# Optimization experiments

Measured on AMD Instinct MI355X. Metric: run time of the kernel, lower is better.

The kernel has to match this reference:

```python
import jax, jax.numpy as jnp
import numpy as np

B, CIN, COUT, H, W = 4, 128, 128, 128, 128
K = 3
K2 = K * K
PAD = 1
EPS = 1e-5


def setup_inputs() -> dict:
    key = jax.random.key(0)
    ks = jax.random.split(key, 11)
    def n(k, shp, s=0.05):
        return jax.random.normal(k, shp, jnp.float32) * s
    return {
        'x': jax.random.normal(ks[0], (B, CIN, H, W), jnp.float32),
        'w_attn': n(ks[1], (COUT, CIN, 3, 3)), 'b_attn': n(ks[2], (COUT,)),
        'w_feat': n(ks[3], (COUT, CIN, 3, 3)), 'b_feat': n(ks[4], (COUT,)),
        'w_org': n(ks[5], (COUT, COUT, 3, 3)), 'b_org': n(ks[6], (COUT,)),
        'w_off': n(ks[7], (2 * K2, COUT, 3, 3), 0.01), 'b_off': n(ks[8], (2 * K2,), 0.01),
        'w_mask': n(ks[9], (K2, COUT, 3, 3)), 'b_mask': n(ks[10], (K2,)),
    }


def _conv(x, w, b, stride=1, pad=1):
    y = jax.lax.conv_general_dilated(
        x, w, (stride, stride), [(pad, pad), (pad, pad)],
        dimension_numbers=('NCHW', 'OIHW', 'NCHW'))
    return y + b[None, :, None, None]


def _instance_norm(x):
    mu = jnp.mean(x, axis=(2, 3), keepdims=True)
    var = jnp.var(x, axis=(2, 3), keepdims=True)
    return (x - mu) * jax.lax.rsqrt(var + EPS)


def _lrelu(x):
    return jnp.where(x > 0, x, 0.2 * x)


def _bilinear_gather(img, y, x):
    Hin, Win = img.shape[2], img.shape[3]
    y0 = jnp.floor(y)
    x0 = jnp.floor(x)
    wy = y - y0
    wx = x - x0
    y0i = y0.astype(jnp.int32)
    x0i = x0.astype(jnp.int32)
    acc = None
    for dy, dx, w in ((0, 0, (1 - wy) * (1 - wx)), (0, 1, (1 - wy) * wx),
                      (1, 0, wy * (1 - wx)), (1, 1, wy * wx)):
        yi = y0i + dy
        xi = x0i + dx
        valid = (yi >= 0) & (yi < Hin) & (xi >= 0) & (xi < Win)
        yc = jnp.clip(yi, 0, Hin - 1)
        xc = jnp.clip(xi, 0, Win - 1)
        g = jax.vmap(lambda im, yy, xx: im[:, yy, xx])(img, yc, xc)  # [B,C,K2,H,W]
        ww = (w * valid.astype(img.dtype))[:, None]
        acc = g * ww if acc is None else acc + g * ww
    return acc


def _deform_conv(x, w_org, b_org, w_off, b_off, w_mask, b_mask):
    # torchvision-style modulated deform_conv2d, K=3, stride=1, pad=1
    b, c, h, w = x.shape
    offset = _conv(x, w_off, b_off, 1, 1)                       # [B,2*K2,H,W]
    mask = jax.nn.sigmoid(_conv(x, w_mask, b_mask, 1, 1))       # [B,K2,H,W]
    off = offset.reshape(b, K2, 2, h, w)
    dy, dx = off[:, :, 0], off[:, :, 1]
    ki = jnp.arange(K2, dtype=jnp.float32) // K                 # tap row (row-major)
    kj = jnp.arange(K2, dtype=jnp.float32) % K                  # tap col
    hh = jnp.arange(h, dtype=jnp.float32)
    wwg = jnp.arange(w, dtype=jnp.float32)
    y = dy + hh[None, None, :, None] + ki[None, :, None, None] - PAD
    xs = dx + wwg[None, None, None, :] + kj[None, :, None, None] - PAD
    samp = _bilinear_gather(x, y, xs)                           # [B,C,K2,H,W]
    samp = samp * mask[:, None]
    wflat = w_org.reshape(w_org.shape[0], c, K2)
    out = jnp.einsum('bckhw,ock->bohw', samp, wflat)
    return out + b_org[None, :, None, None]


def reference(x, w_attn, b_attn, w_feat, b_feat, w_org, b_org,
              w_off, b_off, w_mask, b_mask):
    attn = jax.nn.sigmoid(_conv(x, w_attn, b_attn, 1, 1))
    x_feat = _lrelu(_instance_norm(_conv(x, w_feat, b_feat, 1, 1)))
    x_attned = x_feat * attn
    dconv = _deform_conv(x_attned, w_org, b_org, w_off, b_off, w_mask, b_mask)
    x_valid = _lrelu(_instance_norm(dconv))
    return x_attned + x_valid * (1 - attn)
```

## Files before the change

kernel.cpp:

```cpp
#include <hip/hip_runtime.h>
#include <math.h>

#define BDIM 256
constexpr int BB = 4, Cc = 128, Hh = 128, Wd = 128, HW = Hh * Wd;
constexpr float EPSv = 1e-5f;

typedef __attribute__((ext_vector_type(8))) short short8v;
typedef __attribute__((ext_vector_type(4))) float floatx4;
typedef __attribute__((ext_vector_type(2))) float float2v;

#define MFMA16(a, b, c) __builtin_amdgcn_mfma_f32_16x16x32_bf16((a), (b), (c), 0, 0, 0)

__device__ __forceinline__ float sigmoidf_(float v) { return 1.f / (1.f + __expf(-v)); }

__device__ __forceinline__ unsigned short f2bf(float f) {
    union { float f; unsigned u; } v; v.f = f;
    unsigned r = v.u + 0x7FFFu + ((v.u >> 16) & 1u);
    return (unsigned short)(r >> 16);
}
__device__ __forceinline__ unsigned cvtpk(float a, float b) {
    unsigned r;
    asm("v_cvt_pk_bf16_f32 %0, %1, %2" : "=v"(r) : "v"(a), "v"(b));
    return r;
}
__device__ __forceinline__ float bfu(unsigned short u) { union { unsigned u; float f; } v; v.u = ((unsigned)u) << 16; return v.f; }
__device__ __forceinline__ float2v unpk2(unsigned u) {
    union { unsigned x[2]; float2v f; } v;
    v.x[0] = u << 16;
    v.x[1] = u & 0xFFFF0000u;
    return v.f;
}

__device__ __forceinline__ void barrier_lgkm() {
    asm volatile("s_waitcnt lgkmcnt(0)" ::: "memory");
    __builtin_amdgcn_s_barrier();
}

__device__ __forceinline__ void gload16(const void* g, void* l) {
    __builtin_amdgcn_global_load_lds(
        (const __attribute__((address_space(1))) unsigned int*)g,
        (__attribute__((address_space(3))) unsigned int*)l, 16, 0, 0);
}

__global__ void repack_all_k(const float* __restrict__ w_attn, const float* __restrict__ w_feat,
                             const float* __restrict__ w_org, const float* __restrict__ w_off,
                             const float* __restrict__ w_mask, const float* __restrict__ b_off,
                             const float* __restrict__ b_mask,
                             unsigned short* __restrict__ wpkAF, unsigned short* __restrict__ wpkO,
                             unsigned short* __restrict__ wpkOM, float* __restrict__ bom) {
    int idx = blockIdx.x * BDIM + threadIdx.x;
    const int TOT = 26 * 18432;
    if (idx < TOT) {
        int seg = idx / 18432, rem = idx % 18432;
        int i = rem & 7, lane = (rem >> 3) & 63, tap = (rem >> 9) % 9, chunk = rem / (9 * 512);
        int lco = lane & 15;
        int ci = chunk * 32 + (lane >> 4) * 8 + i;
        float v = 0.f;
        unsigned short* dst;
        int didx;
        if (seg < 16) {
            int cot = seg & 7;
            const float* w = (seg < 8) ? w_attn : w_feat;
            int co = cot * 16 + lco;
            v = w[((size_t)co * Cc + ci) * 9 + tap];
            dst = wpkAF; didx = idx;
        } else if (seg < 24) {
            int co = (seg - 16) * 16 + lco;
            v = w_org[((size_t)co * Cc + ci) * 9 + tap];
            dst = wpkO; didx = idx - 16 * 18432;
        } else {
            int co = (seg - 24) * 16 + lco;
            if (co < 18)      v = w_off[((size_t)co * Cc + ci) * 9 + tap];
            else if (co < 27) v = w_mask[((size_t)(co - 18) * Cc + ci) * 9 + tap];
            dst = wpkOM; didx = idx - 24 * 18432;
        }
        dst[didx] = f2bf(v);
    } else if (idx < TOT + 32) {
        int j = idx - TOT;
        bom[j] = (j < 18) ? b_off[j] : (j < 27 ? b_mask[j - 18] : 0.f);
    }
}

__global__ __launch_bounds__(256) void tobf_k(const float* __restrict__ x,
                                              unsigned short* __restrict__ dst) {
    const int h = blockIdx.x, b = blockIdx.y;
    const int t = threadIdx.x;
    __shared__ unsigned short lt[16][128];
    const int ciq = t >> 4, wg = t & 15;
    const int w = t >> 1, half = t & 1;
    for (int s = 0; s < 8; s++) {
        const float* p = x + ((size_t)(b * 128 + s * 16 + ciq) * HW + h * 128 + wg * 8);
        float4 a = *(const float4*)p;
        float4 c = *(const float4*)(p + 4);
        *(uint4*)&lt[ciq][wg * 8] =
            make_uint4(cvtpk(a.x, a.y), cvtpk(a.z, a.w), cvtpk(c.x, c.y), cvtpk(c.z, c.w));
        __syncthreads();
        unsigned r[4];
#pragma unroll
        for (int k = 0; k < 4; k++) {
            unsigned lo = lt[half * 8 + 2 * k][w];
            unsigned hi = lt[half * 8 + 2 * k + 1][w];
            r[k] = lo | (hi << 16);
        }
        *(uint4*)(dst + ((size_t)b * HW + h * 128 + w) * 128 + s * 16 + half * 8) =
            make_uint4(r[0], r[1], r[2], r[3]);
        __syncthreads();
    }
}

template <int COTPB, int WCO, bool SWZ>
__global__ __launch_bounds__(256, 2) void conv3_k(
    const unsigned short* __restrict__ src, const unsigned short* __restrict__ wpk,
    const float* __restrict__ biasA, const float* __restrict__ biasB,
    int bsplit, int sigsplit,
    unsigned short* __restrict__ out, int ldc, int ch0) {
    constexpr int ROWS = 2;
    constexpr int WPX = 4 / WCO;
    constexpr int PXW = 128 / WPX;
    constexpr int PS = PXW / 16;
    constexpr int HB = 128 / ROWS;

    const int t = threadIdx.x;
    const int lane = t & 63, llo = t & 15, lhi = (t >> 4) & 3;
    const int widu = __builtin_amdgcn_readfirstlane(t >> 6);
    const int wr = widu / WPX, wc = widu % WPX;

    int cbi, h0, b;
    if (SWZ) {
        int n = blockIdx.x;
        int xcd = n & 7, j = n >> 3;
        int g = (j >> 2) * 8 + xcd;
        cbi = j & 3;
        h0 = (g % HB) * ROWS;
        b = g / HB;
    } else {
        cbi = 0;
        h0 = ((int)blockIdx.x % HB) * ROWS;
        b = (int)blockIdx.x / HB;
    }
    const int cotbase = cbi * COTPB + wr * 2;

    __shared__ unsigned short xs[2][4][4][128][8];

    floatx4 acc[2][ROWS][PS];
#pragma unroll
    for (int c = 0; c < 2; c++)
#pragma unroll
        for (int row = 0; row < ROWS; row++)
#pragma unroll
            for (int ps = 0; ps < PS; ps++) acc[c][row][ps] = (floatx4){0.f, 0.f, 0.f, 0.f};

    const unsigned short* srcb = src + ((size_t)b * HW + (size_t)(h0 - 1) * 128) * 128;

    auto stage = [&](int chunk, int buf) {
        const unsigned short* sb = srcb + chunk * 32 + widu * 8;
        unsigned short* db = &xs[buf][widu][0][0][0];
#pragma unroll
        for (int i = 0; i < 8; i++) {
            const unsigned short* g = sb + (size_t)(i * 64 + lane) * 128;
            gload16(g, db + i * 512);
        }
    };

    short8v afrA[9][2], afrB[9][2];
    auto loadafr = [&](int chunk, short8v (*dst)[2]) {
#pragma unroll
        for (int tap = 0; tap < 9; tap++)
#pragma unroll
            for (int c = 0; c < 2; c++)
                dst[tap][c] = *(const short8v*)(wpk +
                    ((((size_t)(cotbase + c) * 4 + chunk) * 9 + tap) * 64 + lane) * 8);
    };

    stage(0, 0);
    loadafr(0, afrA);
    __syncthreads();

    const int wcb = wc * PXW;
#pragma unroll
    for (int chunk = 0; chunk < 4; ++chunk) {
        const int buf = chunk & 1;
        if (chunk < 3) {
            stage(chunk + 1, buf ^ 1);
            loadafr(chunk + 1, (chunk & 1) ? afrA : afrB);
        }
        short8v (*cur)[2] = (chunk & 1) ? afrB : afrA;
#pragma unroll
        for (int rowr = 0; rowr < ROWS + 2; ++rowr) {
            const int hh = h0 - 1 + rowr;
            if ((unsigned)hh < 128u) {
#pragma unroll
                for (int dx = 0; dx < 3; ++dx) {
#pragma unroll
                    for (int ps = 0; ps < PS; ps++) {
                        int colr = wcb + ps * 16 + llo + dx - 1;
                        int colc = min(max(colr, 0), 127);
                        short8v bfv = *(const short8v*)&xs[buf][lhi][rowr][colc][0];
                        if (colr != colc) bfv = (short8v)(short)0;
#pragma unroll
                        for (int row = 0; row < ROWS; ++row) {
                            const int r = rowr - row;
                            if (r >= 0 && r < 3) {
                                const int tap = r * 3 + dx;
#pragma unroll
                                for (int c = 0; c < 2; c++)
                                    acc[c][row][ps] = MFMA16(cur[tap][c], bfv, acc[c][row][ps]);
                            }
                        }
                    }
                }
            }
        }
        __syncthreads();
    }

    const int cbase = cbi * (COTPB * 16);
    const float* bp = (cbase < bsplit) ? biasA : biasB;
    const int bshift = (cbase < bsplit) ? 0 : bsplit;
    const bool dosig = cbase < sigsplit;
#pragma unroll
    for (int c = 0; c < 2; c++)
#pragma unroll
        for (int row = 0; row < ROWS; row++)
#pragma unroll
            for (int ps = 0; ps < PS; ps++)
#pragma unroll
                for (int reg = 0; reg < 4; reg++) {
                    int co = cbase + (wr * 2 + c) * 16 + lhi * 4 + reg;
                    int px = wc * PXW + ps * 16 + llo;
                    float v = acc[c][row][ps][reg] + bp[co - bshift];
                    if (dosig) v = sigmoidf_(v);
                    out[((size_t)b * ldc + ch0 + co) * HW + (h0 + row) * Wd + px] = f2bf(v);
                }
}

__global__ __launch_bounds__(256) void inorm_stats_k(const unsigned short* __restrict__ src,
                                                     float* __restrict__ mu, float* __restrict__ rsig,
                                                     int chTot, int ch0) {
    const int bc = blockIdx.x;
    const int b = bc >> 7, c = bc & 127;
    const unsigned short* p = src + ((size_t)b * chTot + ch0 + c) * HW;
    float s = 0.f, s2 = 0.f;
    for (int i = threadIdx.x; i < HW / 8; i += BDIM) {
        uint4 v = *(const uint4*)(p + (size_t)i * 8);
        float2v a = unpk2(v.x), bb = unpk2(v.y), cc = unpk2(v.z), dd = unpk2(v.w);
        s += a[0] + a[1] + bb[0] + bb[1] + cc[0] + cc[1] + dd[0] + dd[1];
        s2 += a[0] * a[0] + a[1] * a[1] + bb[0] * bb[0] + bb[1] * bb[1]
            + cc[0] * cc[0] + cc[1] * cc[1] + dd[0] * dd[0] + dd[1] * dd[1];
    }
    __shared__ float ss[BDIM], sq[BDIM];
    int t = threadIdx.x;
    ss[t] = s; sq[t] = s2;
    __syncthreads();
    for (int off = BDIM / 2; off > 0; off >>= 1) {
        if (t < off) { ss[t] += ss[t + off]; sq[t] += sq[t + off]; }
        __syncthreads();
    }
    if (t == 0) {
        float m = ss[0] / HW;
        float var = sq[0] / HW - m * m;
        mu[bc] = m;
        rsig[bc] = rsqrtf(var + EPSv);
    }
}

__global__ __launch_bounds__(256) void xattned2_k(const unsigned short* __restrict__ rawAF,
                                                  const float* __restrict__ mu,
                                                  const float* __restrict__ rsig,
                                                  unsigned short* __restrict__ xabfG) {
    const int seg = blockIdx.x, h = blockIdx.y, b = blockIdx.z;
    const int t = threadIdx.x;
    __shared__ unsigned short la[64][128];
    const int px4 = t & 15, cl = t >> 4;
#pragma unroll
    for (int p = 0; p < 8; p++) {
        int c = p * 16 + cl;
        int plane = b * 128 + c;
        size_t pixo = (size_t)h * Wd + seg * 64 + px4 * 4;
        uint2 av = *(const uint2*)(rawAF + ((size_t)b * 256 + c) * HW + pixo);
        uint2 fv = *(const uint2*)(rawAF + ((size_t)b * 256 + 128 + c) * HW + pixo);
        float2v a01 = unpk2(av.x), a23 = unpk2(av.y);
        float2v f01 = unpk2(fv.x), f23 = unpk2(fv.y);
        float m = mu[plane], rs = rsig[plane];
        float vs[4];
        float v;
        v = (f01[0] - m) * rs; v = v > 0.f ? v : 0.2f * v; vs[0] = v * a01[0];
        v = (f01[1] - m) * rs; v = v > 0.f ? v : 0.2f * v; vs[1] = v * a01[1];
        v = (f23[0] - m) * rs; v = v > 0.f ? v : 0.2f * v; vs[2] = v * a23[0];
        v = (f23[1] - m) * rs; v = v > 0.f ? v : 0.2f * v; vs[3] = v * a23[1];
#pragma unroll
        for (int j = 0; j < 4; j++) la[px4 * 4 + j][c] = f2bf(vs[j]);
    }
    __syncthreads();
    const int px = t >> 2, part = t & 3;
    const uint4* lp = (const uint4*)&la[px][part * 32];
    unsigned short* dp = xabfG + ((size_t)b * HW + h * 128 + seg * 64 + px) * 128 + part * 32;
    uint4 v0 = lp[0], v1 = lp[1], v2 = lp[2], v3 = lp[3];
    *(uint4*)dp = v0;
    *(uint4*)(dp + 8) = v1;
    *(uint4*)(dp + 16) = v2;
    *(uint4*)(dp + 24) = v3;
}

__global__ __launch_bounds__(256, 4) void deform_mfma_k(
    const unsigned short* __restrict__ xabfG, const unsigned short* __restrict__ om,
    const unsigned short* __restrict__ wpkO, const float* __restrict__ b_org,
    unsigned short* __restrict__ out, int ldc, int ch0) {
    const int seg = blockIdx.x, h = blockIdx.y, b = blockIdx.z;
    const int t = threadIdx.x;
    const int lane = t & 63, llo = t & 15, lhi = (t >> 4) & 3;
    const int wid = t >> 6;
    const int cb = seg * 32;

    __shared__ unsigned short sv[4][9][32][8];
    __shared__ unsigned xt[2][8 * 6 * 40];

    int prA[2][4];
    float prW[2][4];
    int prT0[2], prOff[2];
    bool prV[2], prOK[2];

    const unsigned short* omb = om + (size_t)b * 32 * HW;
#pragma unroll
    for (int u = 0; u < 2; u++) {
        bool valid;
        int pc;
        if (u == 0) { valid = true; pc = t; }
        else { valid = t < 32; pc = 256 + (t & 31); }
        int tap = pc >> 5, pxl = pc & 31;
        int ww = cb + pxl;
        int pix = h * Wd + ww;
        float dy = bfu(omb[(size_t)(2 * tap) * HW + pix]);
        float dxv = bfu(omb[(size_t)(2 * tap + 1) * HW + pix]);
        float msk = sigmoidf_(bfu(omb[(size_t)(18 + tap) * HW + pix]));
        float yy = dy + (float)(h + tap / 3 - 1);
        float xx = dxv + (float)(ww + tap % 3 - 1);
        float y0f = floorf(yy), x0f = floorf(xx);
        float wy = yy - y0f, wx = xx - x0f;
        int y0 = (int)y0f, x0 = (int)x0f;
#pragma unroll
        for (int c2 = 0; c2 < 4; c2++) {
            int ddy = c2 >> 1, ddx = c2 & 1;
            int yi = y0 + ddy, xi = x0 + ddx;
            bool vc = (yi >= 0) && (yi < Hh) && (xi >= 0) && (xi < Wd);
            int yc = min(max(yi, 0), Hh - 1), xc = min(max(xi, 0), Wd - 1);
            float wt = (ddy ? wy : 1.f - wy) * (ddx ? wx : 1.f - wx);
            prA[u][c2] = yc * Wd + xc;
            prW[u][c2] = vc ? wt * msk : 0.f;
        }
        int ty0 = y0 - (h - 2);
        int tx0 = x0 - (cb - 2);
        prOK[u] = ((unsigned)ty0 <= 4u) && ((unsigned)tx0 <= 38u);
        prT0[u] = ty0 * 40 + tx0;
        prOff[u] = tap * 32 + pxl;
        prV[u] = valid;
    }

    floatx4 acc[2][2];
#pragma unroll
    for (int c = 0; c < 2; c++)
#pragma unroll
        for (int ps = 0; ps < 2; ps++) acc[c][ps] = (floatx4){0.f, 0.f, 0.f, 0.f};

    const unsigned short* xab = xabfG + (size_t)b * HW * 128;
    unsigned short* svf = &sv[0][0][0][0];

    uint4 U[2];

    auto issue_stage = [&](int nc) {
        const int cbase = nc * 16;
#pragma unroll
        for (int it = 0; it < 2; it++) {
            int task = t + it * 256;
            if (task < 480) {
                int col = task % 40;
                int rg = task / 40;
                int row = rg % 6, grp = rg / 6;
                int r = h - 2 + row, cX = cb - 2 + col;
                int rc = min(max(r, 0), Hh - 1), cc = min(max(cX, 0), Wd - 1);
                U[it] = *(const uint4*)(xab + ((size_t)rc * 128 + cc) * 128 + cbase + grp * 8);
            }
        }
    };

    issue_stage(0);

    for (int chunk = 0; chunk < 4; ++chunk) {
#pragma unroll
        for (int half = 0; half < 2; ++half) {
            const int hf = chunk * 2 + half;
            unsigned* xtb = xt[hf & 1];
#pragma unroll
            for (int it = 0; it < 2; it++) {
                int task = t + it * 256;
                if (task < 480) {
                    int col = task % 40;
                    int rg = task / 40;
                    int row = rg % 6, grp = rg / 6;
                    int cell = row * 40 + col;
                    xtb[(grp * 4 + 0) * 240 + cell] = U[it].x;
                    xtb[(grp * 4 + 1) * 240 + cell] = U[it].y;
                    xtb[(grp * 4 + 2) * 240 + cell] = U[it].z;
                    xtb[(grp * 4 + 3) * 240 + cell] = U[it].w;
                }
            }
            if (hf < 7) issue_stage(hf + 1);
            barrier_lgkm();
#pragma unroll
            for (int u = 0; u < 2; u++) {
                if (!prV[u]) continue;
                const float w0 = prW[u][0], w1 = prW[u][1], w2 = prW[u][2], w3 = prW[u][3];
                if (prOK[u]) {
                    const unsigned* xp = xtb + prT0[u];
                    unsigned q[8];
#pragma unroll
                    for (int c2 = 0; c2 < 8; c2++) {
                        unsigned c00 = xp[0], c01 = xp[1];
                        unsigned c10 = xp[40], c11 = xp[41];
                        float2v s = unpk2(c00) * w0 + unpk2(c01) * w1
                                  + unpk2(c10) * w2 + unpk2(c11) * w3;
                        q[c2] = cvtpk(s[0], s[1]);
                        xp += 240;
                    }
                    *(uint4*)(svf + ((size_t)((half * 2 + 0) * 288 + prOff[u]) << 3)) =
                        make_uint4(q[0], q[1], q[2], q[3]);
                    *(uint4*)(svf + ((size_t)((half * 2 + 1) * 288 + prOff[u]) << 3)) =
                        make_uint4(q[4], q[5], q[6], q[7]);
                } else {
                    const int a0 = prA[u][0], a1 = prA[u][1], a2 = prA[u][2], a3 = prA[u][3];
                    const int cch = chunk * 32 + half * 16;
#pragma unroll
                    for (int cg2 = 0; cg2 < 2; cg2++) {
                        unsigned q[4];
#pragma unroll
                        for (int pair = 0; pair < 4; pair++) {
                            int co8 = cch + cg2 * 8 + 2 * pair;
                            unsigned c0 = *(const unsigned*)(xab + (size_t)a0 * 128 + co8);
                            unsigned c1 = *(const unsigned*)(xab + (size_t)a1 * 128 + co8);
                            unsigned c2v = *(const unsigned*)(xab + (size_t)a2 * 128 + co8);
                            unsigned c3 = *(const unsigned*)(xab + (size_t)a3 * 128 + co8);
                            float2v s = unpk2(c0) * w0 + unpk2(c1) * w1
                                      + unpk2(c2v) * w2 + unpk2(c3) * w3;
                            q[pair] = cvtpk(s[0], s[1]);
                        }
                        *(uint4*)(svf + ((size_t)((half * 2 + cg2) * 288 + prOff[u]) << 3)) =
                            make_uint4(q[0], q[1], q[2], q[3]);
                    }
                }
            }
        }
        barrier_lgkm();
#pragma unroll
        for (int tap = 0; tap < 9; ++tap) {
            short8v af[2];
#pragma unroll
            for (int c = 0; c < 2; c++) {
                int cot = wid * 2 + c;
                af[c] = *(const short8v*)(wpkO + ((((size_t)cot * 4 + chunk) * 9 + tap) * 64 + lane) * 8);
            }
            short8v bf[2];
#pragma unroll
            for (int ps = 0; ps < 2; ps++)
                bf[ps] = *(const short8v*)&sv[lhi][tap][ps * 16 + llo][0];
#pragma unroll
            for (int c = 0; c < 2; c++)
#pragma unroll
                for (int ps = 0; ps < 2; ps++)
                    acc[c][ps] = MFMA16(af[c], bf[ps], acc[c][ps]);
        }
    }

#pragma unroll
    for (int c = 0; c < 2; c++)
#pragma unroll
        for (int ps = 0; ps < 2; ps++)
#pragma unroll
            for (int reg = 0; reg < 4; reg++) {
                int co = (wid * 2 + c) * 16 + lhi * 4 + reg;
                int px = cb + ps * 16 + llo;
                out[((size_t)b * ldc + ch0 + co) * HW + h * Wd + px] = f2bf(acc[c][ps][reg] + b_org[co]);
            }
}

__global__ __launch_bounds__(256) void final2_k(const unsigned short* __restrict__ rawAF,
                                                const unsigned short* __restrict__ xabfG,
                                                const float* __restrict__ mu,
                                                const float* __restrict__ rsig,
                                                float* __restrict__ outp) {
    const int seg = blockIdx.x, h = blockIdx.y, b = blockIdx.z;
    const int t = threadIdx.x;
    __shared__ unsigned short la[64][128];
    {
        const int px = t >> 2, part = t & 3;
        const unsigned short* sp = xabfG + ((size_t)b * HW + h * 128 + seg * 64 + px) * 128 + part * 32;
        uint4* lp = (uint4*)&la[px][part * 32];
        lp[0] = *(const uint4*)sp;
        lp[1] = *(const uint4*)(sp + 8);
        lp[2] = *(const uint4*)(sp + 16);
        lp[3] = *(const uint4*)(sp + 24);
    }
    __syncthreads();
    const int px4 = t & 15, cl = t >> 4;
#pragma unroll
    for (int p = 0; p < 8; p++) {
        int c = p * 16 + cl;
        int plane = b * 128 + c;
        size_t pixo = (size_t)h * Wd + seg * 64 + px4 * 4;
        uint2 av = *(const uint2*)(rawAF + ((size_t)b * 256 + c) * HW + pixo);
        uint2 dv = *(const uint2*)(rawAF + ((size_t)b * 256 + 128 + c) * HW + pixo);
        float2v a01 = unpk2(av.x), a23 = unpk2(av.y);
        float2v d01 = unpk2(dv.x), d23 = unpk2(dv.y);
        float m = mu[plane], rs = rsig[plane];
        float4 o;
        float v;
        v = (d01[0] - m) * rs; v = v > 0.f ? v : 0.2f * v; o.x = bfu(la[px4 * 4 + 0][c]) + v * (1.f - a01[0]);
        v = (d01[1] - m) * rs; v = v > 0.f ? v : 0.2f * v; o.y = bfu(la[px4 * 4 + 1][c]) + v * (1.f - a01[1]);
        v = (d23[0] - m) * rs; v = v > 0.f ? v : 0.2f * v; o.z = bfu(la[px4 * 4 + 2][c]) + v * (1.f - a23[0]);
        v = (d23[1] - m) * rs; v = v > 0.f ? v : 0.2f * v; o.w = bfu(la[px4 * 4 + 3][c]) + v * (1.f - a23[1]);
        *(float4*)(outp + (size_t)plane * HW + pixo) = o;
    }
}

extern "C" void kernel_launch(void* const* d_in, const int* in_sizes, int n_in,
                              void* d_out, int out_size, void* d_ws, size_t ws_size,
                              hipStream_t stream) {
    const float* x      = (const float*)d_in[0];
    const float* w_attn = (const float*)d_in[1];
    const float* b_attn = (const float*)d_in[2];
    const float* w_feat = (const float*)d_in[3];
    const float* b_feat = (const float*)d_in[4];
    const float* w_org  = (const float*)d_in[5];
    const float* b_org  = (const float*)d_in[6];
    const float* w_off  = (const float*)d_in[7];
    const float* b_off  = (const float*)d_in[8];
    const float* w_mask = (const float*)d_in[9];
    const float* b_mask = (const float*)d_in[10];
    float* out = (float*)d_out;
    (void)in_sizes; (void)n_in; (void)out_size; (void)ws_size;

    float* ws = (float*)d_ws;
    unsigned short* rawAF = (unsigned short*)ws;
    unsigned short* regionA = (unsigned short*)(ws + (size_t)BB * 256 * HW);
    unsigned short* xbfG  = regionA + 16384;
    const size_t bfElems = (size_t)BB * HW * 128;
    float* offmF = (float*)(regionA + 2 * 16384 + bfElems);
    unsigned short* offm = (unsigned short*)offmF;
    float* tail = offmF + (size_t)BB * 32 * HW;
    unsigned short* wpkAF = (unsigned short*)tail;
    unsigned short* wpkO  = wpkAF + (size_t)16 * 18432;
    unsigned short* wpkOM = wpkO + (size_t)8 * 18432;
    float* bOM = (float*)(wpkOM + (size_t)2 * 18432);
    float* mu1 = bOM + 32;
    float* rs1 = mu1 + 512;
    float* mu2 = rs1 + 512;
    float* rs2 = mu2 + 512;

    repack_all_k<<<(26 * 18432 + 32 + BDIM - 1) / BDIM, BDIM, 0, stream>>>(
        w_attn, w_feat, w_org, w_off, w_mask, b_off, b_mask, wpkAF, wpkO, wpkOM, bOM);

    tobf_k<<<dim3(Hh, BB), BDIM, 0, stream>>>(x, xbfG);

    conv3_k<4, 2, true><<<1024, BDIM, 0, stream>>>(
        xbfG, wpkAF, b_attn, b_feat, 128, 128, rawAF, 256, 0);

    inorm_stats_k<<<BB * Cc, BDIM, 0, stream>>>(rawAF, mu1, rs1, 256, 128);

    xattned2_k<<<dim3(2, Hh, BB), BDIM, 0, stream>>>(rawAF, mu1, rs1, xbfG);

    conv3_k<2, 1, false><<<256, BDIM, 0, stream>>>(
        xbfG, wpkOM, bOM, bOM, 32, 0, offm, 32, 0);

    deform_mfma_k<<<dim3(4, Hh, BB), BDIM, 0, stream>>>(
        xbfG, offm, wpkO, b_org, rawAF, 256, 128);

    inorm_stats_k<<<BB * Cc, BDIM, 0, stream>>>(rawAF, mu2, rs2, 256, 128);

    final2_k<<<dim3(2, Hh, BB), BDIM, 0, stream>>>(rawAF, xbfG, mu2, rs2, out);
}
```

Before: 170.1 us.

## Split offset/mask conv over input-channel chunks with separate reduction kernel

```diff
diff --git a/kernel.cpp b/kernel.cpp
--- a/kernel.cpp
+++ b/kernel.cpp
@@ -234,6 +234,106 @@
                 }
 }
 
+__global__ __launch_bounds__(256, 2) void omsplit_k(
+    const unsigned short* __restrict__ src, const unsigned short* __restrict__ wpk,
+    float* __restrict__ P) {
+    constexpr int ROWS = 2, PXW = 32, PS = 2;
+    const int chunk = blockIdx.x, h0 = (int)blockIdx.y * ROWS, b = blockIdx.z;
+    const int t = threadIdx.x;
+    const int lane = t & 63, llo = t & 15, lhi = (t >> 4) & 3;
+    const int widu = __builtin_amdgcn_readfirstlane(t >> 6);
+    const int wc = widu;
+
+    __shared__ unsigned short xs[4][4][128][8];
+
+    floatx4 acc[2][ROWS][PS];
+#pragma unroll
+    for (int c = 0; c < 2; c++)
+#pragma unroll
+        for (int row = 0; row < ROWS; row++)
+#pragma unroll
+            for (int ps = 0; ps < PS; ps++) acc[c][row][ps] = (floatx4){0.f, 0.f, 0.f, 0.f};
+
+    const unsigned short* srcb = src + ((size_t)b * HW + (size_t)(h0 - 1) * 128) * 128;
+    {
+        const unsigned short* sb = srcb + chunk * 32 + widu * 8;
+        unsigned short* db = &xs[widu][0][0][0];
+#pragma unroll
+        for (int i = 0; i < 8; i++) {
+            const unsigned short* g = sb + (size_t)(i * 64 + lane) * 128;
+            gload16(g, db + i * 512);
+        }
+    }
+    short8v afr[9][2];
+#pragma unroll
+    for (int tap = 0; tap < 9; tap++)
+#pragma unroll
+        for (int c = 0; c < 2; c++)
+            afr[tap][c] = *(const short8v*)(wpk +
+                ((((size_t)c * 4 + chunk) * 9 + tap) * 64 + lane) * 8);
+    __syncthreads();
+
+    const int wcb = wc * PXW;
+#pragma unroll
+    for (int rowr = 0; rowr < ROWS + 2; ++rowr) {
+        const int hh = h0 - 1 + rowr;
+        if ((unsigned)hh < 128u) {
+#pragma unroll
+            for (int dx = 0; dx < 3; ++dx) {
+#pragma unroll
+                for (int ps = 0; ps < PS; ps++) {
+                    int colr = wcb + ps * 16 + llo + dx - 1;
+                    int colc = min(max(colr, 0), 127);
+                    short8v bfv = *(const short8v*)&xs[lhi][rowr][colc][0];
+                    if (colr != colc) bfv = (short8v)(short)0;
+#pragma unroll
+                    for (int row = 0; row < ROWS; ++row) {
+                        const int r = rowr - row;
+                        if (r >= 0 && r < 3) {
+                            const int tap = r * 3 + dx;
+#pragma unroll
+                            for (int c = 0; c < 2; c++)
+                                acc[c][row][ps] = MFMA16(afr[tap][c], bfv, acc[c][row][ps]);
+                        }
+                    }
+                }
+            }
+        }
+    }
+
+    float* Pb = P + (size_t)(chunk * 4 + b) * 32 * HW;
+#pragma unroll
+    for (int c = 0; c < 2; c++)
+#pragma unroll
+        for (int row = 0; row < ROWS; row++)
+#pragma unroll
+            for (int ps = 0; ps < PS; ps++)
+#pragma unroll
+                for (int reg = 0; reg < 4; reg++) {
+                    int co = c * 16 + lhi * 4 + reg;
+                    int px = wcb + ps * 16 + llo;
+                    Pb[(size_t)co * HW + (h0 + row) * Wd + px] = acc[c][row][ps][reg];
+                }
+}
+
+__global__ __launch_bounds__(256) void omreduce_k(const float* __restrict__ P,
+                                                  const float* __restrict__ bom,
+                                                  unsigned short* __restrict__ offm) {
+    const size_t N = (size_t)BB * 32 * HW;
+    size_t i4 = ((size_t)blockIdx.x * BDIM + threadIdx.x) * 4;
+    if (i4 >= N) return;
+    int b = (int)(i4 / (32 * HW));
+    int rem = (int)(i4 % (32 * HW));
+    int co = rem / HW;
+    float4 s = make_float4(bom[co], bom[co], bom[co], bom[co]);
+#pragma unroll
+    for (int chunk = 0; chunk < 4; chunk++) {
+        float4 p = *(const float4*)&P[(size_t)(chunk * 4 + b) * 32 * HW + rem];
+        s.x += p.x; s.y += p.y; s.z += p.z; s.w += p.w;
+    }
+    *(uint2*)(offm + i4) = make_uint2(cvtpk(s.x, s.y), cvtpk(s.z, s.w));
+}
+
 __global__ __launch_bounds__(256) void inorm_stats_k(const unsigned short* __restrict__ src,
                                                      float* __restrict__ mu, float* __restrict__ rsig,
                                                      int chTot, int ch0) {
@@ -540,6 +640,7 @@
 
     float* ws = (float*)d_ws;
     unsigned short* rawAF = (unsigned short*)ws;
+    float* offmP = (float*)(rawAF + (size_t)BB * 256 * HW);
     unsigned short* regionA = (unsigned short*)(ws + (size_t)BB * 256 * HW);
     unsigned short* xbfG  = regionA + 16384;
     const size_t bfElems = (size_t)BB * HW * 128;
@@ -567,8 +668,9 @@
 
     xattned2_k<<<dim3(2, Hh, BB), BDIM, 0, stream>>>(rawAF, mu1, rs1, xbfG);
 
-    conv3_k<2, 1, false><<<256, BDIM, 0, stream>>>(
-        xbfG, wpkOM, bOM, bOM, 32, 0, offm, 32, 0);
+    omsplit_k<<<dim3(4, 64, BB), BDIM, 0, stream>>>(xbfG, wpkOM, offmP);
+    omreduce_k<<<(int)(((size_t)BB * 32 * HW / 4 + BDIM - 1) / BDIM), BDIM, 0, stream>>>(
+        offmP, bOM, offm);
 
     deform_mfma_k<<<dim3(4, Hh, BB), BDIM, 0, stream>>>(
         xbfG, offm, wpkO, b_org, rawAF, 256, 128);
```

After: 179.6 us. 5.5% more time.

## Fuse instance-norm statistics into conv and deform-conv epilogues

Applied to the files above, without the earlier changes.

```diff
diff --git a/kernel.cpp b/kernel.cpp
--- a/kernel.cpp
+++ b/kernel.cpp
@@ -108,12 +108,13 @@
     }
 }
 
-template <int COTPB, int WCO, bool SWZ>
+template <int COTPB, int WCO, bool SWZ, bool STATS>
 __global__ __launch_bounds__(256, 2) void conv3_k(
     const unsigned short* __restrict__ src, const unsigned short* __restrict__ wpk,
     const float* __restrict__ biasA, const float* __restrict__ biasB,
     int bsplit, int sigsplit,
-    unsigned short* __restrict__ out, int ldc, int ch0) {
+    unsigned short* __restrict__ out, int ldc, int ch0,
+    float* __restrict__ S1p, float* __restrict__ S2p) {
     constexpr int ROWS = 2;
     constexpr int WPX = 4 / WCO;
     constexpr int PXW = 128 / WPX;
@@ -218,35 +219,50 @@
     const float* bp = (cbase < bsplit) ? biasA : biasB;
     const int bshift = (cbase < bsplit) ? 0 : bsplit;
     const bool dosig = cbase < sigsplit;
+    const bool dostats = STATS && (cbase >= bsplit);
 #pragma unroll
     for (int c = 0; c < 2; c++)
 #pragma unroll
-        for (int row = 0; row < ROWS; row++)
-#pragma unroll
-            for (int ps = 0; ps < PS; ps++)
-#pragma unroll
-                for (int reg = 0; reg < 4; reg++) {
-                    int co = cbase + (wr * 2 + c) * 16 + lhi * 4 + reg;
-                    int px = wc * PXW + ps * 16 + llo;
-                    float v = acc[c][row][ps][reg] + bp[co - bshift];
+        for (int reg = 0; reg < 4; reg++) {
+            int co = cbase + (wr * 2 + c) * 16 + lhi * 4 + reg;
+            float bv = bp[co - bshift];
+            float s = 0.f, s2 = 0.f;
+#pragma unroll
+            for (int row = 0; row < ROWS; row++)
+#pragma unroll
+                for (int ps = 0; ps < PS; ps++) {
+                    int px = wcb + ps * 16 + llo;
+                    float v = acc[c][row][ps][reg] + bv;
                     if (dosig) v = sigmoidf_(v);
                     out[((size_t)b * ldc + ch0 + co) * HW + (h0 + row) * Wd + px] = f2bf(v);
+                    s += v; s2 += v * v;
                 }
-}
-
-__global__ __launch_bounds__(256) void inorm_stats_k(const unsigned short* __restrict__ src,
-                                                     float* __restrict__ mu, float* __restrict__ rsig,
-                                                     int chTot, int ch0) {
-    const int bc = blockIdx.x;
-    const int b = bc >> 7, c = bc & 127;
-    const unsigned short* p = src + ((size_t)b * chTot + ch0 + c) * HW;
+            if (dostats) {
+#pragma unroll
+                for (int m = 1; m < 16; m <<= 1) {
+                    s += __shfl_xor(s, m, 64);
+                    s2 += __shfl_xor(s2, m, 64);
+                }
+                if (llo == 0) {
+                    int plane = b * 128 + (co - bsplit);
+                    int slot = (h0 / ROWS) * WPX + wc;
+                    S1p[(size_t)plane * (HB * WPX) + slot] = s;
+                    S2p[(size_t)plane * (HB * WPX) + slot] = s2;
+                }
+            }
+        }
+}
+
+__global__ __launch_bounds__(256) void inorm_reduce_k(const float* __restrict__ S1p,
+                                                      const float* __restrict__ S2p,
+                                                      int nslots,
+                                                      float* __restrict__ mu,
+                                                      float* __restrict__ rsig) {
+    const int plane = blockIdx.x;
     float s = 0.f, s2 = 0.f;
-    for (int i = threadIdx.x; i < HW / 8; i += BDIM) {
-        uint4 v = *(const uint4*)(p + (size_t)i * 8);
-        float2v a = unpk2(v.x), bb = unpk2(v.y), cc = unpk2(v.z), dd = unpk2(v.w);
-        s += a[0] + a[1] + bb[0] + bb[1] + cc[0] + cc[1] + dd[0] + dd[1];
-        s2 += a[0] * a[0] + a[1] * a[1] + bb[0] * bb[0] + bb[1] * bb[1]
-            + cc[0] * cc[0] + cc[1] * cc[1] + dd[0] * dd[0] + dd[1] * dd[1];
+    for (int i = threadIdx.x; i < nslots; i += BDIM) {
+        s += S1p[(size_t)plane * nslots + i];
+        s2 += S2p[(size_t)plane * nslots + i];
     }
     __shared__ float ss[BDIM], sq[BDIM];
     int t = threadIdx.x;
@@ -259,8 +275,8 @@
     if (t == 0) {
         float m = ss[0] / HW;
         float var = sq[0] / HW - m * m;
-        mu[bc] = m;
-        rsig[bc] = rsqrtf(var + EPSv);
+        mu[plane] = m;
+        rsig[plane] = rsqrtf(var + EPSv);
     }
 }
 
@@ -305,7 +321,8 @@
 __global__ __launch_bounds__(256, 4) void deform_mfma_k(
     const unsigned short* __restrict__ xabfG, const unsigned short* __restrict__ om,
     const unsigned short* __restrict__ wpkO, const float* __restrict__ b_org,
-    unsigned short* __restrict__ out, int ldc, int ch0) {
+    unsigned short* __restrict__ out, int ldc, int ch0,
+    float* __restrict__ S1d, float* __restrict__ S2d) {
     const int seg = blockIdx.x, h = blockIdx.y, b = blockIdx.z;
     const int t = threadIdx.x;
     const int lane = t & 63, llo = t & 15, lhi = (t >> 4) & 3;
@@ -473,13 +490,28 @@
 #pragma unroll
     for (int c = 0; c < 2; c++)
 #pragma unroll
-        for (int ps = 0; ps < 2; ps++)
-#pragma unroll
-            for (int reg = 0; reg < 4; reg++) {
-                int co = (wid * 2 + c) * 16 + lhi * 4 + reg;
+        for (int reg = 0; reg < 4; reg++) {
+            int co = (wid * 2 + c) * 16 + lhi * 4 + reg;
+            float bv = b_org[co];
+            float s = 0.f, s2 = 0.f;
+#pragma unroll
+            for (int ps = 0; ps < 2; ps++) {
                 int px = cb + ps * 16 + llo;
-                out[((size_t)b * ldc + ch0 + co) * HW + h * Wd + px] = f2bf(acc[c][ps][reg] + b_org[co]);
-            }
+                float v = acc[c][ps][reg] + bv;
+                out[((size_t)b * ldc + ch0 + co) * HW + h * Wd + px] = f2bf(v);
+                s += v; s2 += v * v;
+            }
+#pragma unroll
+            for (int m = 1; m < 16; m <<= 1) {
+                s += __shfl_xor(s, m, 64);
+                s2 += __shfl_xor(s2, m, 64);
+            }
+            if (llo == 0) {
+                int plane = b * 128 + co;
+                S1d[(size_t)plane * 512 + h * 4 + seg] = s;
+                S2d[(size_t)plane * 512 + h * 4 + seg] = s2;
+            }
+        }
 }
 
 __global__ __launch_bounds__(256) void final2_k(const unsigned short* __restrict__ rawAF,
@@ -554,26 +586,30 @@
     float* rs1 = mu1 + 512;
     float* mu2 = rs1 + 512;
     float* rs2 = mu2 + 512;
+    float* S1a = rs2 + 512;
+    float* S2a = S1a + 512 * 128;
+    float* S1d = S2a + 512 * 128;
+    float* S2d = S1d + 512 * 512;
 
     repack_all_k<<<(26 * 18432 + 32 + BDIM - 1) / BDIM, BDIM, 0, stream>>>(
         w_attn, w_feat, w_org, w_off, w_mask, b_off, b_mask, wpkAF, wpkO, wpkOM, bOM);
 
     tobf_k<<<dim3(Hh, BB), BDIM, 0, stream>>>(x, xbfG);
 
-    conv3_k<4, 2, true><<<1024, BDIM, 0, stream>>>(
-        xbfG, wpkAF, b_attn, b_feat, 128, 128, rawAF, 256, 0);
-
-    inorm_stats_k<<<BB * Cc, BDIM, 0, stream>>>(rawAF, mu1, rs1, 256, 128);
+    conv3_k<4, 2, true, true><<<1024, BDIM, 0, stream>>>(
+        xbfG, wpkAF, b_attn, b_feat, 128, 128, rawAF, 256, 0, S1a, S2a);
+
+    inorm_reduce_k<<<512, BDIM, 0, stream>>>(S1a, S2a, 128, mu1, rs1);
 
     xattned2_k<<<dim3(2, Hh, BB), BDIM, 0, stream>>>(rawAF, mu1, rs1, xbfG);
 
-    conv3_k<2, 1, false><<<256, BDIM, 0, stream>>>(
-        xbfG, wpkOM, bOM, bOM, 32, 0, offm, 32, 0);
+    conv3_k<2, 1, false, false><<<256, BDIM, 0, stream>>>(
+        xbfG, wpkOM, bOM, bOM, 32, 0, offm, 32, 0, nullptr, nullptr);
 
     deform_mfma_k<<<dim3(4, Hh, BB), BDIM, 0, stream>>>(
-        xbfG, offm, wpkO, b_org, rawAF, 256, 128);
-
-    inorm_stats_k<<<BB * Cc, BDIM, 0, stream>>>(rawAF, mu2, rs2, 256, 128);
+        xbfG, offm, wpkO, b_org, rawAF, 256, 128, S1d, S2d);
+
+    inorm_reduce_k<<<512, BDIM, 0, stream>>>(S1d, S2d, 512, mu2, rs2);
 
     final2_k<<<dim3(2, Hh, BB), BDIM, 0, stream>>>(rawAF, xbfG, mu2, rs2, out);
 }
```

Result: slower. 177.0 us (+4.0%).
